# Kernel tuning notes

Hardware: AMD Instinct MI355X
Metric: run time of the kernel (lower is better)

## Reference

```python
import math
import jax, jax.numpy as jnp
import numpy as np

N_HEAD = 16

def skew(QEr):
    # QEr: (B, H, L, L) where last dim indexes relative positions via Er_t
    B, H, L, _ = QEr.shape
    padded = jnp.pad(QEr, ((0, 0), (0, 0), (0, 0), (1, 0)))        # (B,H,L,L+1)
    reshaped = padded.reshape(B, H, L + 1, L)                       # (B,H,L+1,L)
    return reshaped[:, :, 1:, :]                                    # (B,H,L,L)

def setup_inputs() -> dict:
    key = jax.random.key(0)
    ks = jax.random.split(key, 6)
    B, L, D = 2, 2048, 1024
    hs = D // N_HEAD
    block_size = 2048
    return {
        "x": jax.random.normal(ks[0], (B, L, D), dtype=jnp.float32),
        "W_attn": jax.random.normal(ks[1], (D, 3 * D), dtype=jnp.float32) * 0.02,
        "b_attn": jnp.zeros((3 * D,), dtype=jnp.float32),
        "W_proj": jax.random.normal(ks[2], (D, D), dtype=jnp.float32) * 0.02,
        "b_proj": jnp.zeros((D,), dtype=jnp.float32),
        "Er": jax.random.normal(ks[3], (block_size, hs), dtype=jnp.float32),
    }

def reference(x, W_attn, b_attn, W_proj, b_proj, Er):
    B, L, D = x.shape
    H = N_HEAD
    hs = D // H
    qkv = x @ W_attn + b_attn                                       # (B,L,3D)
    q, k, v = jnp.split(qkv, 3, axis=-1)
    q = q.reshape(B, L, H, hs).transpose(0, 2, 1, 3)                # (B,H,L,hs)
    k = k.reshape(B, L, H, hs).transpose(0, 2, 1, 3)
    v = v.reshape(B, L, H, hs).transpose(0, 2, 1, 3)
    start = Er.shape[0] - L
    Er_t = Er[start:, :].T                                          # (hs,L)
    QEr = jnp.einsum('bhld,de->bhle', q, Er_t)                      # (B,H,L,L)
    Srel = skew(QEr)
    QK_t = jnp.einsum('bhqd,bhkd->bhqk', q, k)
    scale = 1.0 / math.sqrt(hs)
    att = (QK_t + Srel) * scale
    causal = jnp.tril(jnp.ones((L, L), dtype=bool))
    att = jnp.where(causal[None, None, :, :], att, -jnp.inf)
    att = jax.nn.softmax(att, axis=-1)
    y = jnp.einsum('bhqk,bhkd->bhqd', att, v)                       # (B,H,L,hs)
    y = y.transpose(0, 2, 1, 3).reshape(B, L, D)
    return y @ W_proj + b_proj
```

## Files before the change

### kernel.cpp

```cpp
#include <hip/hip_runtime.h>
#include <stdint.h>

#define L_SEQ 2048
#define D_MODEL 1024
#define NHEAD 16
#define HS 64
#define B_BATCH 2
#define QSCALE 0.1803368801111243f

typedef __bf16 bf16x8 __attribute__((ext_vector_type(8)));
typedef float f32x4 __attribute__((ext_vector_type(4)));

__device__ __forceinline__ float fexp2(float x) {
  return __builtin_amdgcn_exp2f(x);
}

__device__ __forceinline__ unsigned short f2b(float f) {
  unsigned int u = __float_as_uint(f);
  u += 0x7fffu + ((u >> 16) & 1u);
  return (unsigned short)(u >> 16);
}
__device__ __forceinline__ unsigned int pk2(float a, float b) {
  return (unsigned int)f2b(a) | ((unsigned int)f2b(b) << 16);
}
__device__ __forceinline__ unsigned int cvtpk(float a, float b) {
  unsigned int r;
  asm("v_cvt_pk_bf16_f32 %0, %1, %2" : "=v"(r) : "v"(a), "v"(b));
  return r;
}

union U8 { uint4 v; unsigned short s[8]; };

__device__ __forceinline__ void ldsload16(const unsigned short* g, unsigned short* l) {
  __builtin_amdgcn_global_load_lds(
      (const __attribute__((address_space(1))) unsigned int*)g,
      (__attribute__((address_space(3))) unsigned int*)l, 16, 0, 0);
}

__device__ __forceinline__ bf16x8 frag_ld(const unsigned short* base, int row, int ks, int quad) {
  const int unit = (ks * 4 + quad) ^ (row & 7);
  return *(const bf16x8*)(base + row * 64 + unit * 8);
}

__global__ __launch_bounds__(256) void prep(
    const float* __restrict__ x, const float* __restrict__ Wa,
    const float* __restrict__ Wp, const float* __restrict__ Er,
    unsigned short* __restrict__ xb, unsigned short* __restrict__ wabT,
    unsigned short* __restrict__ wpbT, unsigned short* __restrict__ erb) {
  __shared__ unsigned short tt[64][65];
  int gb = blockIdx.x;
  if (gb < 2048) {
    int i = gb * 256 + threadIdx.x;
    const float4* s4 = (const float4*)x;
    float4 a = s4[i * 2], b = s4[i * 2 + 1];
    U8 u;
    u.s[0] = f2b(a.x); u.s[1] = f2b(a.y); u.s[2] = f2b(a.z); u.s[3] = f2b(a.w);
    u.s[4] = f2b(b.x); u.s[5] = f2b(b.y); u.s[6] = f2b(b.z); u.s[7] = f2b(b.w);
    ((uint4*)xb)[i] = u.v;
    return;
  }
  gb -= 2048;
  if (gb < 68) {
    int i = gb * 256 + threadIdx.x;
    if (i < 16384) {
      const float4* s4 = (const float4*)Er;
      float4 a = s4[i * 2], b = s4[i * 2 + 1];
      U8 u;
      u.s[0] = f2b(a.x); u.s[1] = f2b(a.y); u.s[2] = f2b(a.z); u.s[3] = f2b(a.w);
      u.s[4] = f2b(b.x); u.s[5] = f2b(b.y); u.s[6] = f2b(b.z); u.s[7] = f2b(b.w);
      ((uint4*)erb)[i] = u.v;
    } else {
      ((uint4*)erb)[i] = make_uint4(0u, 0u, 0u, 0u);
    }
    return;
  }
  gb -= 68;
  const float* src;
  unsigned short* dst;
  int N, nbx;
  if (gb < 768) { src = Wa; dst = wabT; N = 3072; nbx = 48; }
  else { gb -= 768; src = Wp; dst = wpbT; N = 1024; nbx = 16; }
  const int n0 = (gb % nbx) * 64, k0 = (gb / nbx) * 64;
  const int c = threadIdx.x & 63, r0 = threadIdx.x >> 6;
#pragma unroll
  for (int i = 0; i < 16; i++) {
    int r = r0 * 16 + i;
    tt[r][c] = f2b(src[(size_t)(k0 + r) * N + n0 + c]);
  }
  __syncthreads();
  const int n = threadIdx.x >> 2, ks = (threadIdx.x & 3) * 16;
  U8 u0, u1;
#pragma unroll
  for (int j = 0; j < 8; j++) {
    u0.s[j] = tt[ks + j][n];
    u1.s[j] = tt[ks + 8 + j][n];
  }
  unsigned short* d = dst + (size_t)(n0 + n) * 1024 + k0 + ks;
  *(uint4*)d = u0.v;
  *(uint4*)(d + 8) = u1.v;
}

__global__ __launch_bounds__(256, 3) void gemm_qkv(
    const unsigned short* __restrict__ A, const unsigned short* __restrict__ Bt,
    const float* __restrict__ bias, unsigned short* __restrict__ qbuf,
    unsigned short* __restrict__ kbuf, unsigned short* __restrict__ vbufT,
    int M, int N, int K) {
  __shared__ unsigned short As[128 * 64];
  __shared__ unsigned short Bs[128 * 64];
  const int tid = threadIdx.x, lane = tid & 63, w = tid >> 6;
  const int wm = w >> 1, wn = w & 1, quad = lane >> 4, lc = lane & 15;
  const int wgid = blockIdx.x;
  const int xcd = wgid & 7, t = wgid >> 3;
  const int bnr = t % 3, bm = t / 3;
  const int bn = xcd * 3 + bnr;
  const int l8 = lane >> 3, u8 = ((lane & 7) ^ l8) * 8;
  const unsigned short* Ab = A + (size_t)bm * 128 * K;
  const unsigned short* Bb = Bt + (size_t)bn * 128 * K;

  f32x4 z4 = {0.f, 0.f, 0.f, 0.f};
  f32x4 acc[4][4];
#pragma unroll
  for (int mb = 0; mb < 4; mb++)
#pragma unroll
    for (int nb = 0; nb < 4; nb++) acc[mb][nb] = z4;

  for (int kk = 0; kk < K; kk += 64) {
    if (kk) __syncthreads();
#pragma unroll
    for (int i = 0; i < 4; i++) {
      int ch = w * 4 + i;
      ldsload16(Ab + (size_t)(ch * 8 + l8) * K + kk + u8, &As[ch * 512]);
      ldsload16(Bb + (size_t)(ch * 8 + l8) * K + kk + u8, &Bs[ch * 512]);
    }
    __syncthreads();
#pragma unroll
    for (int ks = 0; ks < 2; ks++) {
      bf16x8 af[4], bfv[4];
#pragma unroll
      for (int mb = 0; mb < 4; mb++) af[mb] = frag_ld(As, wm * 64 + mb * 16 + lc, ks, quad);
#pragma unroll
      for (int nb = 0; nb < 4; nb++) bfv[nb] = frag_ld(Bs, wn * 64 + nb * 16 + lc, ks, quad);
#pragma unroll
      for (int mb = 0; mb < 4; mb++)
#pragma unroll
        for (int nb = 0; nb < 4; nb++)
          acc[mb][nb] = __builtin_amdgcn_mfma_f32_16x16x32_bf16(af[mb], bfv[nb],
                                                               acc[mb][nb], 0, 0, 0);
    }
  }

#pragma unroll
  for (int nb = 0; nb < 4; nb++) {
    const int n = bn * 128 + wn * 64 + nb * 16 + lc;
    const float bv = bias[n];
    const int which = n >> 10;
    const int rem = n & 1023;
    const int h = rem >> 6, d = rem & 63;
#pragma unroll
    for (int mb = 0; mb < 4; mb++) {
      const int m0 = bm * 128 + wm * 64 + mb * 16 + quad * 4;
      const int b = m0 >> 11, l0 = m0 & 2047;
      if (which == 2) {
        float v0 = acc[mb][nb][0] + bv, v1 = acc[mb][nb][1] + bv;
        float v2 = acc[mb][nb][2] + bv, v3 = acc[mb][nb][3] + bv;
        uint2 pv;
        pv.x = pk2(v0, v1);
        pv.y = pk2(v2, v3);
        *(uint2*)&vbufT[((size_t)(b * NHEAD + h) * HS + d) * L_SEQ + l0] = pv;
      } else {
        const float sc = which == 0 ? QSCALE : 1.0f;
        unsigned short* dst = (which == 0) ? qbuf : kbuf;
#pragma unroll
        for (int reg = 0; reg < 4; reg++) {
          float val = (acc[mb][nb][reg] + bv) * sc;
          dst[((size_t)(b * NHEAD + h) * L_SEQ + l0 + reg) * HS + d] = f2b(val);
        }
      }
    }
  }
}

__global__ __launch_bounds__(256, 3) void gemm_proj(
    const unsigned short* __restrict__ A, const unsigned short* __restrict__ Bt,
    const float* __restrict__ bias, float* __restrict__ out, int M, int N, int K) {
  __shared__ unsigned short As[128 * 64];
  __shared__ unsigned short Bs[64 * 64];
  const int tid = threadIdx.x, lane = tid & 63, w = tid >> 6;
  const int quad = lane >> 4, lc = lane & 15;
  const int wgid = blockIdx.x;
  const int xcd = wgid & 7, t = wgid >> 3;
  const int bnr = t & 1, bm = t >> 1;
  const int bn = xcd * 2 + bnr;
  const int l8 = lane >> 3, u8 = ((lane & 7) ^ l8) * 8;
  const unsigned short* Ab = A + (size_t)bm * 128 * K;
  const unsigned short* Bb = Bt + (size_t)bn * 64 * K;

  f32x4 z4 = {0.f, 0.f, 0.f, 0.f};
  f32x4 acc[2][4];
#pragma unroll
  for (int mb = 0; mb < 2; mb++)
#pragma unroll
    for (int nb = 0; nb < 4; nb++) acc[mb][nb] = z4;

  for (int kk = 0; kk < K; kk += 64) {
    if (kk) __syncthreads();
#pragma unroll
    for (int i = 0; i < 4; i++) {
      int ch = w * 4 + i;
      ldsload16(Ab + (size_t)(ch * 8 + l8) * K + kk + u8, &As[ch * 512]);
    }
#pragma unroll
    for (int i = 0; i < 2; i++) {
      int ch = w * 2 + i;
      ldsload16(Bb + (size_t)(ch * 8 + l8) * K + kk + u8, &Bs[ch * 512]);
    }
    __syncthreads();
#pragma unroll
    for (int ks = 0; ks < 2; ks++) {
      bf16x8 af[2], bfv[4];
#pragma unroll
      for (int mb = 0; mb < 2; mb++) af[mb] = frag_ld(As, w * 32 + mb * 16 + lc, ks, quad);
#pragma unroll
      for (int nb = 0; nb < 4; nb++) bfv[nb] = frag_ld(Bs, nb * 16 + lc, ks, quad);
#pragma unroll
      for (int mb = 0; mb < 2; mb++)
#pragma unroll
        for (int nb = 0; nb < 4; nb++)
          acc[mb][nb] = __builtin_amdgcn_mfma_f32_16x16x32_bf16(af[mb], bfv[nb],
                                                               acc[mb][nb], 0, 0, 0);
    }
  }

#pragma unroll
  for (int nb = 0; nb < 4; nb++) {
    const int n = bn * 64 + nb * 16 + lc;
    const float bv = bias[n];
#pragma unroll
    for (int mb = 0; mb < 2; mb++) {
#pragma unroll
      for (int reg = 0; reg < 4; reg++) {
        const int m = bm * 128 + w * 32 + mb * 16 + quad * 4 + reg;
        out[(size_t)m * N + n] = acc[mb][nb][reg] + bv;
      }
    }
  }
}

__global__ __launch_bounds__(256, 3) void flash_attn_rel(
    const unsigned short* __restrict__ qb, const unsigned short* __restrict__ kb,
    const unsigned short* __restrict__ vbT, const unsigned short* __restrict__ erb,
    unsigned short* __restrict__ yb) {
  __shared__ unsigned short Ks[64 * 64];
  __shared__ unsigned short Vt[64 * 64];
  __shared__ unsigned short Es[128 * 64];
  __shared__ float Twf[4][16 * 84];

  const int tid = threadIdx.x, lane = tid & 63, w = tid >> 6;
  const int quad = lane >> 4, lc = lane & 15;
  const int wgid = blockIdx.x;
  const int xcd = wgid & 7, r7 = wgid >> 3;
  const int bhr = r7 & 3, y = r7 >> 2;
  const int bh = xcd * 4 + bhr;
  const int b = bh >> 4, h = bh & 15;
  const int qt = 31 - y;
  const int q0 = qt * 64;
  const int qg0 = q0 + w * 16;
  const size_t hoff = (size_t)bh * L_SEQ * HS;
  float* TwfW = Twf[w];
  unsigned short* TwpW = (unsigned short*)TwfW;
  const int l8 = lane >> 3, u8 = ((lane & 7) ^ l8) * 8;
  const f32x4 z4 = {0.f, 0.f, 0.f, 0.f};

  bf16x8 qf[2];
  {
    const unsigned short* qrow = qb + hoff + (size_t)(qg0 + lc) * HS;
    qf[0] = *(const bf16x8*)(qrow + quad * 8);
    qf[1] = *(const bf16x8*)(qrow + 32 + quad * 8);
  }
  f32x4 Oacc[4];
#pragma unroll
  for (int db = 0; db < 4; db++) Oacc[db] = z4;
  float psum_acc = 0.0f;

  const unsigned short* kgb = kb + hoff;
  const unsigned short* vgbT = vbT + (size_t)bh * HS * L_SEQ;
  const int ebw = 48 - w * 16;
  const int e_anchor = (L_SEQ - 64) - q0;

  for (int k0 = 0; k0 <= q0; k0 += 64) {
    __syncthreads();
#pragma unroll
    for (int i = 0; i < 2; i++) {
      int ch = w * 2 + i;
      ldsload16(kgb + (size_t)(k0 + ch * 8 + l8) * HS + u8, &Ks[ch * 512]);
      ldsload16(vgbT + (size_t)(ch * 8 + l8) * L_SEQ + k0 + u8, &Vt[ch * 512]);
    }
    if (k0 == 0) {
#pragma unroll
      for (int i = 0; i < 4; i++) {
        int ch = w * 4 + i;
        ldsload16(erb + (size_t)(e_anchor + ch * 8 + l8) * HS + u8, &Es[ch * 512]);
      }
    } else {
#pragma unroll
      for (int i = 0; i < 2; i++) {
        int ch = w * 2 + i;
        const int er = k0 + 64 + ch * 8;
        ldsload16(erb + (size_t)(e_anchor + er + l8) * HS + u8,
                  &Es[(er & 127) * 64]);
      }
    }
    __syncthreads();

    f32x4 sacc[4], tacc[5];
#pragma unroll
    for (int i = 0; i < 4; i++) sacc[i] = z4;
#pragma unroll
    for (int i = 0; i < 5; i++) tacc[i] = z4;
    const int eb0 = k0 + ebw;
    __builtin_amdgcn_s_setprio(1);
#pragma unroll
    for (int ks = 0; ks < 2; ks++) {
#pragma unroll
      for (int kbi = 0; kbi < 4; kbi++) {
        bf16x8 a = frag_ld(Ks, kbi * 16 + lc, ks, quad);
        sacc[kbi] = __builtin_amdgcn_mfma_f32_16x16x32_bf16(a, qf[ks], sacc[kbi], 0, 0, 0);
      }
#pragma unroll
      for (int eb = 0; eb < 5; eb++) {
        bf16x8 a = frag_ld(Es, (eb0 + eb * 16 + lc) & 127, ks, quad);
        tacc[eb] = __builtin_amdgcn_mfma_f32_16x16x32_bf16(a, qf[ks], tacc[eb], 0, 0, 0);
      }
    }
    __builtin_amdgcn_s_setprio(0);
#pragma unroll
    for (int eb = 0; eb < 5; eb++)
      *(f32x4*)&TwfW[lc * 84 + eb * 16 + quad * 4] = tacc[eb];
    asm volatile("" ::: "memory");

    float p[4][4], ps = 0.0f;
    const int tbase = lc * 84 + (15 - lc);
    if (k0 == q0) {
      const int qrow = w * 16 + lc;
#pragma unroll
      for (int kbi = 0; kbi < 4; kbi++)
#pragma unroll
        for (int reg = 0; reg < 4; reg++) {
          const int kk = kbi * 16 + quad * 4 + reg;
          float t = TwfW[tbase + kk];
          float v = (kk > qrow) ? -1e30f : (sacc[kbi][reg] + t);
          p[kbi][reg] = fexp2(v);
          ps += p[kbi][reg];
        }
    } else {
#pragma unroll
      for (int kbi = 0; kbi < 4; kbi++)
#pragma unroll
        for (int reg = 0; reg < 4; reg++) {
          float t = TwfW[tbase + kbi * 16 + quad * 4 + reg];
          p[kbi][reg] = fexp2(sacc[kbi][reg] + t);
          ps += p[kbi][reg];
        }
    }
    psum_acc += ps;
#pragma unroll
    for (int kbi = 0; kbi < 4; kbi++) {
      uint2 pk;
      pk.x = cvtpk(p[kbi][0], p[kbi][1]);
      pk.y = cvtpk(p[kbi][2], p[kbi][3]);
      const int k = kbi * 16 + quad * 4;
      *(uint2*)&TwpW[lc * 64 + (((k >> 3) ^ (lc & 7)) << 3) + (k & 7)] = pk;
    }
    asm volatile("" ::: "memory");

    __builtin_amdgcn_s_setprio(1);
#pragma unroll
    for (int ks = 0; ks < 2; ks++) {
      bf16x8 pf = frag_ld(TwpW, lc, ks, quad);
#pragma unroll
      for (int db = 0; db < 4; db++) {
        bf16x8 av = frag_ld(Vt, db * 16 + lc, ks, quad);
        Oacc[db] = __builtin_amdgcn_mfma_f32_16x16x32_bf16(av, pf, Oacc[db], 0, 0, 0);
      }
    }
    __builtin_amdgcn_s_setprio(0);
  }

  psum_acc += __shfl_xor(psum_acc, 16, 64);
  psum_acc += __shfl_xor(psum_acc, 32, 64);
  const float inv = 1.0f / psum_acc;

  __syncthreads();
  unsigned short* Yt = Es;
#pragma unroll
  for (int db = 0; db < 4; db++) {
    uint2 pk;
    pk.x = cvtpk(Oacc[db][0] * inv, Oacc[db][1] * inv);
    pk.y = cvtpk(Oacc[db][2] * inv, Oacc[db][3] * inv);
    *(uint2*)&Yt[(w * 16 + lc) * 72 + db * 16 + quad * 4] = pk;
  }
  __syncthreads();
  {
    const int r = tid >> 2, seg = (tid & 3) * 16;
    uint4 a0 = *(const uint4*)&Yt[r * 72 + seg];
    uint4 a1 = *(const uint4*)&Yt[r * 72 + seg + 8];
    unsigned short* d = yb + (size_t)((size_t)b * L_SEQ + q0 + r) * D_MODEL + h * HS + seg;
    *(uint4*)d = a0;
    *(uint4*)(d + 8) = a1;
  }
}

extern "C" void kernel_launch(void* const* d_in, const int* in_sizes, int n_in,
                              void* d_out, int out_size, void* d_ws, size_t ws_size,
                              hipStream_t stream) {
  const float* x = (const float*)d_in[0];
  const float* W_attn = (const float*)d_in[1];
  const float* b_attn = (const float*)d_in[2];
  const float* W_proj = (const float*)d_in[3];
  const float* b_proj = (const float*)d_in[4];
  const float* Er = (const float*)d_in[5];
  float* out = (float*)d_out;

  const int n_x = B_BATCH * L_SEQ * D_MODEL;
  const int n_wa = D_MODEL * 3 * D_MODEL;
  const int n_wp = D_MODEL * D_MODEL;
  const int n_er_pad = (L_SEQ + 128) * HS;
  const int n_head = B_BATCH * NHEAD * L_SEQ * HS;

  unsigned short* xb = (unsigned short*)d_ws;
  unsigned short* wabT = xb + n_x;
  unsigned short* wpbT = wabT + n_wa;
  unsigned short* erb = wpbT + n_wp;
  unsigned short* qbuf = erb + n_er_pad;
  unsigned short* kbuf = qbuf + n_head;
  unsigned short* vbufT = kbuf + n_head;
  unsigned short* ybuf = vbufT + n_head;

  prep<<<3140, 256, 0, stream>>>(x, W_attn, W_proj, Er, xb, wabT, wpbT, erb);

  gemm_qkv<<<768, 256, 0, stream>>>(xb, wabT, b_attn, qbuf, kbuf, vbufT,
                                    B_BATCH * L_SEQ, 3 * D_MODEL, D_MODEL);

  flash_attn_rel<<<1024, 256, 0, stream>>>(qbuf, kbuf, vbufT, erb, ybuf);

  gemm_proj<<<512, 256, 0, stream>>>(ybuf, wpbT, b_proj, out,
                                     B_BATCH * L_SEQ, D_MODEL, D_MODEL);
}
```

Baseline: 189.8 us.

## Rewrite QKV GEMM with 256x256 tiles, 8 waves, double-buffered LDS pipeline

The QKV projection GEMM moves from 128x128 tiles with 4 waves and single-buffered LDS to 256x256 tiles with 8 waves and 128KB of dynamic LDS split into two buffers. Global-to-LDS staging of the next k-tile is interleaved with MFMA work, using fine-grained waitcnt and barriers plus raised wave priority around the MFMA blocks. A new XCD-aware block swizzle maps the 192 workgroups to tiles. The aim is to hide load latency and raise data reuse per tile, at the cost of fewer workgroups (192 on a 256-CU part), lower occupancy and higher register pressure.

```diff
diff --git a/kernel.cpp b/kernel.cpp
--- a/kernel.cpp
+++ b/kernel.cpp
@@ -100,69 +100,140 @@
   *(uint4*)(d + 8) = u1.v;
 }
 
-__global__ __launch_bounds__(256, 3) void gemm_qkv(
+__global__ __launch_bounds__(512, 2) void gemm_qkv(
     const unsigned short* __restrict__ A, const unsigned short* __restrict__ Bt,
     const float* __restrict__ bias, unsigned short* __restrict__ qbuf,
     unsigned short* __restrict__ kbuf, unsigned short* __restrict__ vbufT,
     int M, int N, int K) {
-  __shared__ unsigned short As[128 * 64];
-  __shared__ unsigned short Bs[128 * 64];
+  extern __shared__ unsigned short SH[];
   const int tid = threadIdx.x, lane = tid & 63, w = tid >> 6;
-  const int wm = w >> 1, wn = w & 1, quad = lane >> 4, lc = lane & 15;
-  const int wgid = blockIdx.x;
-  const int xcd = wgid & 7, t = wgid >> 3;
-  const int bnr = t % 3, bm = t / 3;
-  const int bn = xcd * 3 + bnr;
+  const int wm = w >> 2, wn = w & 3, quad = lane >> 4, lc = lane & 15;
+  const int wgid = (int)blockIdx.x;
+  const int swz = (wgid & 7) * 24 + (wgid >> 3);
+  const int bm = swz / 12, bn = swz % 12;
   const int l8 = lane >> 3, u8 = ((lane & 7) ^ l8) * 8;
-  const unsigned short* Ab = A + (size_t)bm * 128 * K;
-  const unsigned short* Bb = Bt + (size_t)bn * 128 * K;
-
-  f32x4 z4 = {0.f, 0.f, 0.f, 0.f};
-  f32x4 acc[4][4];
-#pragma unroll
-  for (int mb = 0; mb < 4; mb++)
-#pragma unroll
-    for (int nb = 0; nb < 4; nb++) acc[mb][nb] = z4;
-
-  for (int kk = 0; kk < K; kk += 64) {
-    if (kk) __syncthreads();
-#pragma unroll
-    for (int i = 0; i < 4; i++) {
-      int ch = w * 4 + i;
-      ldsload16(Ab + (size_t)(ch * 8 + l8) * K + kk + u8, &As[ch * 512]);
-      ldsload16(Bb + (size_t)(ch * 8 + l8) * K + kk + u8, &Bs[ch * 512]);
-    }
-    __syncthreads();
-#pragma unroll
-    for (int ks = 0; ks < 2; ks++) {
-      bf16x8 af[4], bfv[4];
-#pragma unroll
-      for (int mb = 0; mb < 4; mb++) af[mb] = frag_ld(As, wm * 64 + mb * 16 + lc, ks, quad);
-#pragma unroll
-      for (int nb = 0; nb < 4; nb++) bfv[nb] = frag_ld(Bs, wn * 64 + nb * 16 + lc, ks, quad);
-#pragma unroll
-      for (int mb = 0; mb < 4; mb++)
-#pragma unroll
-        for (int nb = 0; nb < 4; nb++)
-          acc[mb][nb] = __builtin_amdgcn_mfma_f32_16x16x32_bf16(af[mb], bfv[nb],
-                                                               acc[mb][nb], 0, 0, 0);
-    }
-  }
-
-#pragma unroll
-  for (int nb = 0; nb < 4; nb++) {
-    const int n = bn * 128 + wn * 64 + nb * 16 + lc;
+  const int nkt = K >> 6;
+  const unsigned short* Agb = A + (size_t)bm * 256 * K;
+  const unsigned short* Bgb = Bt + (size_t)bn * 256 * K;
+  unsigned short* SA = SH;
+  unsigned short* SB = SH + 32768;
+
+  f32x4 acc[8][4];
+  {
+    const f32x4 z4 = {0.f, 0.f, 0.f, 0.f};
+#pragma unroll
+    for (int mf = 0; mf < 8; mf++)
+#pragma unroll
+      for (int nf = 0; nf < 4; nf++) acc[mf][nf] = z4;
+  }
+
+  auto stgA = [&](int kt, int h) {
+    if (kt >= nkt) return;
+    unsigned short* d = SA + (kt & 1) * 16384 + h * 8192;
+    const int c0 = w * 2, r0 = h * 128;
+    ldsload16(Agb + (size_t)(r0 + c0 * 8 + l8) * K + kt * 64 + u8, d + c0 * 512);
+    ldsload16(Agb + (size_t)(r0 + (c0 + 1) * 8 + l8) * K + kt * 64 + u8, d + (c0 + 1) * 512);
+  };
+  auto stgB = [&](int kt, int h) {
+    if (kt >= nkt) return;
+    unsigned short* d = SB + (kt & 1) * 16384 + h * 8192;
+    const int c0 = w * 2, r0 = h * 128;
+    ldsload16(Bgb + (size_t)(r0 + c0 * 8 + l8) * K + kt * 64 + u8, d + c0 * 512);
+    ldsload16(Bgb + (size_t)(r0 + (c0 + 1) * 8 + l8) * K + kt * 64 + u8, d + (c0 + 1) * 512);
+  };
+
+#define LOADA(BUF, KS)                                                        \
+  _Pragma("unroll") for (int mf_ = 0; mf_ < 8; mf_++)                         \
+      af[mf_] = frag_ld((BUF), wm * 128 + mf_ * 16 + lc, (KS), quad);
+
+#define MMA2(B0_, B1_, NFA, NFB)                                              \
+  __builtin_amdgcn_s_setprio(1);                                              \
+  _Pragma("unroll") for (int mf_ = 0; mf_ < 8; mf_++) {                       \
+    acc[mf_][NFA] = __builtin_amdgcn_mfma_f32_16x16x32_bf16(af[mf_], (B0_),   \
+                                                            acc[mf_][NFA], 0, 0, 0); \
+    acc[mf_][NFB] = __builtin_amdgcn_mfma_f32_16x16x32_bf16(af[mf_], (B1_),   \
+                                                            acc[mf_][NFB], 0, 0, 0); \
+  }                                                                           \
+  __builtin_amdgcn_s_setprio(0);
+
+#define SYNC_L()  asm volatile("s_waitcnt lgkmcnt(0)" ::: "memory"); \
+                  __builtin_amdgcn_s_barrier();
+#define SYNC_LV() asm volatile("s_waitcnt vmcnt(2) lgkmcnt(0)" ::: "memory"); \
+                  __builtin_amdgcn_s_barrier();
+
+  stgA(0, 0); stgA(0, 1); stgB(0, 0); stgB(0, 1); stgA(1, 0);
+  asm volatile("s_waitcnt vmcnt(2)" ::: "memory");
+  __builtin_amdgcn_s_barrier();
+
+  bf16x8 af[8], b0, b1, b2, b3;
+  const unsigned short* A0 = SA;
+  const unsigned short* A1 = SA + 16384;
+  const unsigned short* B0 = SB;
+  const unsigned short* B1 = SB + 16384;
+  const int r0b = wn * 64 + lc;
+
+  for (int t = 0; t < (nkt >> 1); ++t) {
+    const int kb = 2 * t + 1, kn = 2 * t + 2;
+    LOADA(A0, 0);
+    b0 = frag_ld(B0, r0b, 0, quad);
+    b1 = frag_ld(B0, r0b + 16, 0, quad);
+    stgA(kb, 1);
+    SYNC_L();
+    MMA2(b0, b1, 0, 1);
+    b2 = frag_ld(B0, r0b + 32, 0, quad);
+    b3 = frag_ld(B0, r0b + 48, 0, quad);
+    stgB(kb, 0);
+    SYNC_L();
+    MMA2(b2, b3, 2, 3);
+    LOADA(A0, 1);
+    b0 = frag_ld(B0, r0b, 1, quad);
+    b1 = frag_ld(B0, r0b + 16, 1, quad);
+    stgB(kb, 1);
+    SYNC_L();
+    MMA2(b0, b1, 0, 1);
+    b2 = frag_ld(B0, r0b + 32, 1, quad);
+    b3 = frag_ld(B0, r0b + 48, 1, quad);
+    stgA(kn, 0);
+    SYNC_LV();
+    MMA2(b2, b3, 2, 3);
+    LOADA(A1, 0);
+    b0 = frag_ld(B1, r0b, 0, quad);
+    b1 = frag_ld(B1, r0b + 16, 0, quad);
+    stgA(kn, 1);
+    SYNC_L();
+    MMA2(b0, b1, 0, 1);
+    b2 = frag_ld(B1, r0b + 32, 0, quad);
+    b3 = frag_ld(B1, r0b + 48, 0, quad);
+    stgB(kn, 0);
+    SYNC_L();
+    MMA2(b2, b3, 2, 3);
+    LOADA(A1, 1);
+    b0 = frag_ld(B1, r0b, 1, quad);
+    b1 = frag_ld(B1, r0b + 16, 1, quad);
+    stgB(kn, 1);
+    SYNC_L();
+    MMA2(b0, b1, 0, 1);
+    b2 = frag_ld(B1, r0b + 32, 1, quad);
+    b3 = frag_ld(B1, r0b + 48, 1, quad);
+    stgA(kn + 1, 0);
+    SYNC_LV();
+    MMA2(b2, b3, 2, 3);
+  }
+
+#pragma unroll
+  for (int nf = 0; nf < 4; nf++) {
+    const int n = bn * 256 + wn * 64 + nf * 16 + lc;
     const float bv = bias[n];
     const int which = n >> 10;
     const int rem = n & 1023;
     const int h = rem >> 6, d = rem & 63;
 #pragma unroll
-    for (int mb = 0; mb < 4; mb++) {
-      const int m0 = bm * 128 + wm * 64 + mb * 16 + quad * 4;
+    for (int mf = 0; mf < 8; mf++) {
+      const int m0 = bm * 256 + wm * 128 + mf * 16 + quad * 4;
       const int b = m0 >> 11, l0 = m0 & 2047;
       if (which == 2) {
-        float v0 = acc[mb][nb][0] + bv, v1 = acc[mb][nb][1] + bv;
-        float v2 = acc[mb][nb][2] + bv, v3 = acc[mb][nb][3] + bv;
+        float v0 = acc[mf][nf][0] + bv, v1 = acc[mf][nf][1] + bv;
+        float v2 = acc[mf][nf][2] + bv, v3 = acc[mf][nf][3] + bv;
         uint2 pv;
         pv.x = pk2(v0, v1);
         pv.y = pk2(v2, v3);
@@ -172,12 +243,16 @@
         unsigned short* dst = (which == 0) ? qbuf : kbuf;
 #pragma unroll
         for (int reg = 0; reg < 4; reg++) {
-          float val = (acc[mb][nb][reg] + bv) * sc;
+          float val = (acc[mf][nf][reg] + bv) * sc;
           dst[((size_t)(b * NHEAD + h) * L_SEQ + l0 + reg) * HS + d] = f2b(val);
         }
       }
     }
   }
+#undef LOADA
+#undef MMA2
+#undef SYNC_L
+#undef SYNC_LV
 }
 
 __global__ __launch_bounds__(256, 3) void gemm_proj(
@@ -438,8 +513,8 @@
 
   prep<<<3140, 256, 0, stream>>>(x, W_attn, W_proj, Er, xb, wabT, wpbT, erb);
 
-  gemm_qkv<<<768, 256, 0, stream>>>(xb, wabT, b_attn, qbuf, kbuf, vbufT,
-                                    B_BATCH * L_SEQ, 3 * D_MODEL, D_MODEL);
+  gemm_qkv<<<192, 512, 131072, stream>>>(xb, wabT, b_attn, qbuf, kbuf, vbufT,
+                                         B_BATCH * L_SEQ, 3 * D_MODEL, D_MODEL);
 
   flash_attn_rel<<<1024, 256, 0, stream>>>(qbuf, kbuf, vbufT, erb, ybuf);
 
```

New measurement: 230.7 us. +21.6%, slower.
